# Performance work log

Measured on AMD Instinct MI355X. Metric: run time of the kernel, lower is better.

Reference implementation:

```python
import jax, jax.numpy as jnp
import numpy as np

EPS = 1e-5


def _bn(v, gamma, beta, mean, var):
    # v: [n, c, L, 1]; per-channel eval-mode batchnorm
    scale = gamma / jnp.sqrt(var + EPS)
    return v * scale[None, :, None, None] + (beta - mean * scale)[None, :, None, None]


def _conv1x1(v, w, b):
    # v: [n, c, L, 1], w: [o, c], b: [o] -> [n, o, L, 1]
    y = jnp.einsum('ncl,oc->nol', v[..., 0], w) + b[None, :, None]
    return y[..., None]


def setup_inputs() -> dict:
    key = jax.random.key(0)
    ks = jax.random.split(key, 16)
    N, C, H, W, MIP = 8, 256, 112, 112, 8
    return {
        'x': jax.random.normal(ks[0], (N, C, H, W), dtype=jnp.float32),
        'bn1_gamma': jax.random.uniform(ks[1], (C,), dtype=jnp.float32),
        'bn1_beta': jax.random.normal(ks[2], (C,), dtype=jnp.float32) * 0.1,
        'bn1_mean': jax.random.normal(ks[3], (C,), dtype=jnp.float32) * 0.1,
        'bn1_var': jax.random.uniform(ks[4], (C,), dtype=jnp.float32) + 0.5,
        'bn2_gamma': jax.random.uniform(ks[5], (C,), dtype=jnp.float32),
        'bn2_beta': jax.random.normal(ks[6], (C,), dtype=jnp.float32) * 0.1,
        'bn2_mean': jax.random.normal(ks[7], (C,), dtype=jnp.float32) * 0.1,
        'bn2_var': jax.random.uniform(ks[8], (C,), dtype=jnp.float32) + 0.5,
        'ds_w': jax.random.normal(ks[9], (MIP, C), dtype=jnp.float32) * (1.0 / np.sqrt(C)),
        'ds_b': jax.random.normal(ks[10], (MIP,), dtype=jnp.float32) * 0.01,
        'us_w': jax.random.normal(ks[11], (C, MIP), dtype=jnp.float32) * (1.0 / np.sqrt(MIP)),
        'us_b': jax.random.normal(ks[12], (C,), dtype=jnp.float32) * 0.01,
    }


def reference(x, bn1_gamma, bn1_beta, bn1_mean, bn1_var,
              bn2_gamma, bn2_beta, bn2_mean, bn2_var,
              ds_w, ds_b, us_w, us_b):
    identity = x
    # dual-axis average pooling
    x_h = jnp.mean(x, axis=3, keepdims=True)                 # [n, c, h, 1]
    x_w = jnp.mean(x, axis=2, keepdims=True).transpose(0, 1, 3, 2)  # [n, c, w, 1]
    # batchnorm (eval mode)
    x_h = _bn(x_h, bn1_gamma, bn1_beta, bn1_mean, bn1_var)
    x_w = _bn(x_w, bn2_gamma, bn2_beta, bn2_mean, bn2_var)
    # channel-reduce 1x1 conv + relu
    d_h = jax.nn.relu(_conv1x1(x_h, ds_w, ds_b))             # [n, mip, h, 1]
    d_w = jax.nn.relu(_conv1x1(x_w, ds_w, ds_b))             # [n, mip, w, 1]
    # channel-expand 1x1 conv + sigmoid
    a_h = jax.nn.sigmoid(_conv1x1(d_h, us_w, us_b))          # [n, c, h, 1]
    a_w = jax.nn.sigmoid(_conv1x1(d_w, us_w, us_b))          # [n, c, w, 1]
    a_w = a_w.transpose(0, 1, 3, 2)                          # [n, c, 1, w]
    out = identity * a_w * a_h + identity
    # h_swish: x * relu6(x + 3) / 6
    return out * jnp.clip(out + 3.0, 0.0, 6.0) * (1.0 / 6.0)
```

## Files before the change

kernel.cpp:

```cpp
#include <hip/hip_runtime.h>
#include <math.h>

#define NN 8
#define CC 256
#define HH 112
#define WW 112
#define MIP 8
#define EPS 1e-5f


#define TSTRIDE 113
__global__ __launch_bounds__(256) void pool_kernel(const float* __restrict__ x,
                                                   float* __restrict__ pool) {
    __shared__ float tile[HH * TSTRIDE];
    const int b = blockIdx.x;
    const int n = b / CC;
    const int c = b % CC;
    const int tid = threadIdx.x;

    const float4* p4 = (const float4*)(x + (size_t)b * (HH * WW));
#pragma unroll 4
    for (int i = tid; i < HH * (WW / 4); i += 256) {
        float4 v = p4[i];
        const int h = i / (WW / 4);
        const int w4 = i % (WW / 4);
        float* d = &tile[h * TSTRIDE + w4 * 4];
        d[0] = v.x; d[1] = v.y; d[2] = v.z; d[3] = v.w;
    }
    __syncthreads();

    if (tid < HH) {
        float s = 0.f;
#pragma unroll 8
        for (int w = 0; w < WW; ++w) s += tile[tid * TSTRIDE + w];
        pool[((size_t)(n * HH + tid)) * CC + c] = s * (1.0f / WW);
    } else if (tid >= 128 && tid < 128 + WW) {
        const int w = tid - 128;
        float s = 0.f;
#pragma unroll 8
        for (int h = 0; h < HH; ++h) s += tile[h * TSTRIDE + w];
        pool[(size_t)(NN * HH * CC) + ((size_t)(n * WW + w)) * CC + c] = s * (1.0f / HH);
    }
}

__global__ __launch_bounds__(256) void att_kernel(
    float* __restrict__ pool,
    const float* __restrict__ bn1_g, const float* __restrict__ bn1_b,
    const float* __restrict__ bn1_m, const float* __restrict__ bn1_v,
    const float* __restrict__ bn2_g, const float* __restrict__ bn2_b,
    const float* __restrict__ bn2_m, const float* __restrict__ bn2_v,
    const float* __restrict__ ds_w, const float* __restrict__ ds_b,
    const float* __restrict__ us_w, const float* __restrict__ us_b) {
    __shared__ float s[CC];
    __shared__ float dsh[MIP];

    const int branch = blockIdx.y;
    const int c = threadIdx.x;

    const float* g  = branch ? bn2_g : bn1_g;
    const float* be = branch ? bn2_b : bn1_b;
    const float* mn = branch ? bn2_m : bn1_m;
    const float* vr = branch ? bn2_v : bn1_v;

    const size_t idx = (size_t)branch * (NN * HH * CC) + (size_t)blockIdx.x * CC + c;

    float v = pool[idx];
    float scale = g[c] * rsqrtf(vr[c] + EPS);
    float vb = v * scale + (be[c] - mn[c] * scale);
    s[c] = vb;
    __syncthreads();

    {
        const int grp = c >> 5;
        const int l = c & 31;
        float partial = 0.f;
#pragma unroll
        for (int k = 0; k < CC / 32; ++k) {
            const int cc = l + k * 32;
            partial += ds_w[grp * CC + cc] * s[cc];
        }
#pragma unroll
        for (int off = 16; off > 0; off >>= 1)
            partial += __shfl_down(partial, off, 32);
        if (l == 0) dsh[grp] = fmaxf(partial + ds_b[grp], 0.f);
    }
    __syncthreads();

    float acc = us_b[c];
#pragma unroll
    for (int m = 0; m < MIP; ++m) acc += us_w[c * MIP + m] * dsh[m];
    pool[idx] = 1.0f / (1.0f + expf(-acc));
}

__global__ __launch_bounds__(256) void apply_kernel(const float* __restrict__ x,
                                                    const float* __restrict__ att,
                                                    float* __restrict__ out) {
    __shared__ float ah[HH];
    __shared__ float aw[WW];
    const int b = blockIdx.x;
    const int n = b / CC;
    const int c = b % CC;
    const int tid = threadIdx.x;

    if (tid < HH) {
        ah[tid] = att[((size_t)(n * HH + tid)) * CC + c];
    } else if (tid >= 128 && tid < 128 + WW) {
        const int w = tid - 128;
        aw[w] = att[(size_t)(NN * HH * CC) + ((size_t)(n * WW + w)) * CC + c];
    }
    __syncthreads();

    const float4* xp = (const float4*)(x + (size_t)b * (HH * WW));
    float4* op = (float4*)(out + (size_t)b * (HH * WW));
#pragma unroll 4
    for (int i = tid; i < HH * (WW / 4); i += 256) {
        const int h = i / (WW / 4);
        const int w4 = i % (WW / 4);
        float4 xv = xp[i];
        const float a_h = ah[h];
        float4 o;
        o.x = xv.x * (aw[w4 * 4 + 0] * a_h) + xv.x;
        o.y = xv.y * (aw[w4 * 4 + 1] * a_h) + xv.y;
        o.z = xv.z * (aw[w4 * 4 + 2] * a_h) + xv.z;
        o.w = xv.w * (aw[w4 * 4 + 3] * a_h) + xv.w;
        float4 r;
        r.x = o.x * fminf(fmaxf(o.x + 3.0f, 0.0f), 6.0f) * (1.0f / 6.0f);
        r.y = o.y * fminf(fmaxf(o.y + 3.0f, 0.0f), 6.0f) * (1.0f / 6.0f);
        r.z = o.z * fminf(fmaxf(o.z + 3.0f, 0.0f), 6.0f) * (1.0f / 6.0f);
        r.w = o.w * fminf(fmaxf(o.w + 3.0f, 0.0f), 6.0f) * (1.0f / 6.0f);
        op[i] = r;
    }
}

extern "C" void kernel_launch(void* const* d_in, const int* in_sizes, int n_in,
                              void* d_out, int out_size, void* d_ws, size_t ws_size,
                              hipStream_t stream) {
    const float* x     = (const float*)d_in[0];
    const float* bn1_g = (const float*)d_in[1];
    const float* bn1_b = (const float*)d_in[2];
    const float* bn1_m = (const float*)d_in[3];
    const float* bn1_v = (const float*)d_in[4];
    const float* bn2_g = (const float*)d_in[5];
    const float* bn2_b = (const float*)d_in[6];
    const float* bn2_m = (const float*)d_in[7];
    const float* bn2_v = (const float*)d_in[8];
    const float* ds_w  = (const float*)d_in[9];
    const float* ds_b  = (const float*)d_in[10];
    const float* us_w  = (const float*)d_in[11];
    const float* us_b  = (const float*)d_in[12];
    float* out = (float*)d_out;
    float* pool = (float*)d_ws;

    pool_kernel<<<NN * CC, 256, 0, stream>>>(x, pool);
    att_kernel<<<dim3(NN * HH, 2), 256, 0, stream>>>(pool,
        bn1_g, bn1_b, bn1_m, bn1_v, bn2_g, bn2_b, bn2_m, bn2_v,
        ds_w, ds_b, us_w, us_b);
    apply_kernel<<<NN * CC, 256, 0, stream>>>(x, pool, out);
}
```

Measured before the change: 225.0 us.

## Reduce pooling in registers with small partial tiles; use nontemporal loads/stores in apply

The pooling kernel no longer stages the whole 112x112 plane in shared memory. Each thread accumulates row sums and column partial sums in registers over strided rows and writes only small partial arrays, which cuts LDS traffic and footprint and so allows more blocks per CU. The apply kernel now uses nontemporal loads and stores for x and out to avoid polluting the cache with streaming data. One risk is that the nontemporal load of x may stop it from being served out of cache after the pool pass reads it.

```diff
diff --git a/kernel.cpp b/kernel.cpp
--- a/kernel.cpp
+++ b/kernel.cpp
@@ -8,37 +8,46 @@
 #define MIP 8
 #define EPS 1e-5f
 
+typedef float nvec4 __attribute__((ext_vector_type(4)));
 
-#define TSTRIDE 113
+
 __global__ __launch_bounds__(256) void pool_kernel(const float* __restrict__ x,
                                                    float* __restrict__ pool) {
-    __shared__ float tile[HH * TSTRIDE];
+    __shared__ float rowpart[HH][29];
+    __shared__ float4 colpart[8][28];
     const int b = blockIdx.x;
     const int n = b / CC;
     const int c = b % CC;
-    const int tid = threadIdx.x;
+    const int t = threadIdx.x;
 
     const float4* p4 = (const float4*)(x + (size_t)b * (HH * WW));
-#pragma unroll 4
-    for (int i = tid; i < HH * (WW / 4); i += 256) {
-        float4 v = p4[i];
-        const int h = i / (WW / 4);
-        const int w4 = i % (WW / 4);
-        float* d = &tile[h * TSTRIDE + w4 * 4];
-        d[0] = v.x; d[1] = v.y; d[2] = v.z; d[3] = v.w;
+
+    if (t < 224) {
+        const int g = t / 28;
+        const int j = t % 28;
+        float4 ca = make_float4(0.f, 0.f, 0.f, 0.f);
+#pragma unroll
+        for (int k = 0; k < 14; ++k) {
+            const int r = g + 8 * k;
+            float4 v = p4[r * 28 + j];
+            ca.x += v.x; ca.y += v.y; ca.z += v.z; ca.w += v.w;
+            rowpart[r][j] = v.x + v.y + v.z + v.w;
+        }
+        colpart[g][j] = ca;
     }
     __syncthreads();
 
-    if (tid < HH) {
+    if (t < HH) {
         float s = 0.f;
-#pragma unroll 8
-        for (int w = 0; w < WW; ++w) s += tile[tid * TSTRIDE + w];
-        pool[((size_t)(n * HH + tid)) * CC + c] = s * (1.0f / WW);
-    } else if (tid >= 128 && tid < 128 + WW) {
-        const int w = tid - 128;
+#pragma unroll
+        for (int j = 0; j < 28; ++j) s += rowpart[t][j];
+        pool[((size_t)(n * HH + t)) * CC + c] = s * (1.0f / WW);
+    } else if (t < 112 + WW) {
+        const int w = t - 112;
+        const float* cp = (const float*)&colpart[0][0];
         float s = 0.f;
-#pragma unroll 8
-        for (int h = 0; h < HH; ++h) s += tile[h * TSTRIDE + w];
+#pragma unroll
+        for (int g = 0; g < 8; ++g) s += cp[g * 112 + w];
         pool[(size_t)(NN * HH * CC) + ((size_t)(n * WW + w)) * CC + c] = s * (1.0f / HH);
     }
 }
@@ -110,25 +119,25 @@
     }
     __syncthreads();
 
-    const float4* xp = (const float4*)(x + (size_t)b * (HH * WW));
-    float4* op = (float4*)(out + (size_t)b * (HH * WW));
+    const nvec4* xp = (const nvec4*)(x + (size_t)b * (HH * WW));
+    nvec4* op = (nvec4*)(out + (size_t)b * (HH * WW));
 #pragma unroll 4
     for (int i = tid; i < HH * (WW / 4); i += 256) {
         const int h = i / (WW / 4);
         const int w4 = i % (WW / 4);
-        float4 xv = xp[i];
+        nvec4 xv = __builtin_nontemporal_load(&xp[i]);
         const float a_h = ah[h];
-        float4 o;
+        nvec4 o;
         o.x = xv.x * (aw[w4 * 4 + 0] * a_h) + xv.x;
         o.y = xv.y * (aw[w4 * 4 + 1] * a_h) + xv.y;
         o.z = xv.z * (aw[w4 * 4 + 2] * a_h) + xv.z;
         o.w = xv.w * (aw[w4 * 4 + 3] * a_h) + xv.w;
-        float4 r;
+        nvec4 r;
         r.x = o.x * fminf(fmaxf(o.x + 3.0f, 0.0f), 6.0f) * (1.0f / 6.0f);
         r.y = o.y * fminf(fmaxf(o.y + 3.0f, 0.0f), 6.0f) * (1.0f / 6.0f);
         r.z = o.z * fminf(fmaxf(o.z + 3.0f, 0.0f), 6.0f) * (1.0f / 6.0f);
         r.w = o.w * fminf(fmaxf(o.w + 3.0f, 0.0f), 6.0f) * (1.0f / 6.0f);
-        op[i] = r;
+        __builtin_nontemporal_store(r, &op[i]);
     }
 }
 
```

Result: no change. 224.8 us (-0.1%).
